# Performance work log

Measured on AMD Instinct MI355X. Metric: run time of the kernel, lower is better.

## Reference

```python
import jax, jax.numpy as jnp
import numpy as np

B, T, C = 4, 2048, 1024
NH = 16
HD = C // NH  # 64


def setup_inputs() -> dict:
    key = jax.random.key(0)
    k1, k2, k3 = jax.random.split(key, 3)
    x = jax.random.normal(k1, (B, T, C), dtype=jnp.float32)
    # causal mask buffer, 1 = keep, 0 = mask out
    mask = jnp.tril(jnp.ones((T, T), dtype=jnp.int32))[None, None, :, :]
    # learned params (Linear with bias=False): torch stores weight as [out, in],
    # y = x @ W.T ; we store transposed for direct matmul
    w_qkv = jax.random.normal(k2, (C, 3 * C), dtype=jnp.float32) / np.sqrt(C)
    w_proj = jax.random.normal(k3, (C, C), dtype=jnp.float32) / np.sqrt(C)
    return {"x": x, "mask": mask, "w_qkv": w_qkv, "w_proj": w_proj}


def reference(x, mask, w_qkv, w_proj):
    b, t, c = x.shape
    qkv = x @ w_qkv  # [b, t, 3c]
    q, k, v = jnp.split(qkv, 3, axis=-1)
    # [b, nh, t, hd]
    q = q.reshape(b, t, NH, HD).transpose(0, 2, 1, 3)
    k = k.reshape(b, t, NH, HD).transpose(0, 2, 1, 3)
    v = v.reshape(b, t, NH, HD).transpose(0, 2, 1, 3)
    att = jnp.einsum("bhqd,bhkd->bhqk", q, k) * (1.0 / np.sqrt(HD))
    att = jnp.where(mask == 0, -jnp.inf, att)
    att = jax.nn.softmax(att, axis=-1)
    y = jnp.einsum("bhqk,bhkd->bhqd", att, v)
    y = y.transpose(0, 2, 1, 3).reshape(b, t, c)
    return y @ w_proj
```

## Files before the change

### kernel.cpp

```cpp
#include <hip/hip_runtime.h>
#include <hip/hip_bf16.h>

typedef _Float16 f16;
typedef __attribute__((ext_vector_type(2))) __fp16 fp16x2;
typedef __attribute__((ext_vector_type(4))) _Float16 f16x4;
typedef __attribute__((ext_vector_type(8))) _Float16 f16x8;
typedef __attribute__((ext_vector_type(4))) float f32x4;

#define MFMA16(a, b, c) __builtin_amdgcn_mfma_f32_16x16x16f16((a), (b), (c), 0, 0, 0)
#define MFMA32(a, b, c) __builtin_amdgcn_mfma_f32_16x16x32_f16((a), (b), (c), 0, 0, 0)
#define EXP2(x) __builtin_amdgcn_exp2f(x)
#define GLOAD_LDS16(g, l)                                                        \
  __builtin_amdgcn_global_load_lds((const __attribute__((address_space(1))) void*)(g), \
                                   (__attribute__((address_space(3))) void*)(l), 16, 0, 0)
typedef const __attribute__((address_space(3))) char* lds_cp;
#define TR16(dst, addr, imm) \
  asm volatile("ds_read_b64_tr_b16 %0, %1 offset:" imm : "=v"(dst) : "v"(addr))

__global__ __launch_bounds__(256) void prep_kernel(
    const float* __restrict__ x, f16* __restrict__ x16,
    const float* __restrict__ wq, f16* __restrict__ wqT,
    const float* __restrict__ wp, f16* __restrict__ wpT) {
  const int blk = blockIdx.x;
  const int tid = threadIdx.x;
  if (blk < 8192) {
    int i = blk * 256 + tid;
    const float4 v = reinterpret_cast<const float4*>(x)[i];
    f16x4 h;
    h[0] = (f16)v.x; h[1] = (f16)v.y; h[2] = (f16)v.z; h[3] = (f16)v.w;
    reinterpret_cast<f16x4*>(x16)[i] = h;
    return;
  }
  const float* src;
  f16* dst;
  int R, Cc, bx, by;
  if (blk < 11264) {
    int j = blk - 8192;
    bx = j % 96; by = j / 96;
    src = wq; dst = wqT; R = 1024; Cc = 3072;
  } else {
    int j = blk - 11264;
    bx = j & 31; by = j >> 5;
    src = wp; dst = wpT; R = 1024; Cc = 1024;
  }
  __shared__ float t[32][33];
  int tx0 = bx * 32, ty0 = by * 32;
  int c = tid & 31;
  int r0 = tid >> 5;
#pragma unroll
  for (int i = 0; i < 4; i++) {
    int r = r0 + 8 * i;
    t[r][c] = src[(size_t)(ty0 + r) * Cc + tx0 + c];
  }
  __syncthreads();
#pragma unroll
  for (int i = 0; i < 4; i++) {
    int a = r0 + 8 * i;
    dst[(size_t)(tx0 + a) * R + ty0 + c] = (f16)t[c][a];
  }
}

__global__ __launch_bounds__(512, 2) void gemm_qkv_kernel(
    const f16* __restrict__ A, const f16* __restrict__ Bt, f16* __restrict__ C,
    int M, int N, int K) {
  __shared__ __align__(16) char smem[163840];
  const int tid = threadIdx.x;
  const int lane = tid & 63, wid = tid >> 6;
  const int wm = wid >> 2, wn = wid & 3;
  const int lo = lane & 15, hi = lane >> 4;

  const int ntn = N / 384;
  const int nwg = (M >> 8) * ntn;
  const int wg = (blockIdx.x & 7) * (nwg >> 3) + (blockIdx.x >> 3);
  const int tm0 = (wg / ntn) << 8;
  const int tn0 = (wg % ntn) * 384;

  const int prow = tid >> 3;
  const int u8 = (tid & 7) ^ (prow & 7);
  const f16* a0 = A + (size_t)(tm0 + prow) * K + u8 * 8;
  const f16* b0 = Bt + (size_t)(tn0 + prow) * K + u8 * 8;

  const int swz = lo & 7;
  const int as0 = (hi ^ swz) << 4, as1 = ((4 + hi) ^ swz) << 4;
  const int abase = (wm * 128 + lo) * 128;
  const int bbase = 32768 + (wn * 96 + lo) * 128;

  f32x4 acc[8][6] = {};

  auto stage = [&](int ke, char* buf) {
#pragma unroll
    for (int c = 0; c < 4; c++)
      GLOAD_LDS16(a0 + (size_t)c * 64 * K + ke, buf + c * 8192 + tid * 16);
#pragma unroll
    for (int c = 0; c < 6; c++)
      GLOAD_LDS16(b0 + (size_t)c * 64 * K + ke, buf + 32768 + c * 8192 + tid * 16);
  };

  const int NT = K >> 6;
  stage(0, smem);

  for (int t = 0; t < NT; t++) {
    char* db = smem + (t & 1) * 81920;
    asm volatile("s_waitcnt vmcnt(0)" ::: "memory");
    __builtin_amdgcn_s_barrier();
    if (t + 1 < NT) stage((t + 1) << 6, smem + ((t + 1) & 1) * 81920);
    __builtin_amdgcn_sched_barrier(0);

#pragma unroll
    for (int ks = 0; ks < 2; ks++) {
      const int so = ks ? as1 : as0;
      f16x8 b[6];
#pragma unroll
      for (int ni = 0; ni < 6; ni++)
        b[ni] = *(const f16x8*)(db + bbase + ni * 2048 + so);
      __builtin_amdgcn_s_setprio(1);
#pragma unroll
      for (int mi = 0; mi < 8; mi++) {
        f16x8 a = *(const f16x8*)(db + abase + mi * 2048 + so);
#pragma unroll
        for (int ni = 0; ni < 6; ni++)
          acc[mi][ni] = MFMA32(a, b[ni], acc[mi][ni]);
      }
      __builtin_amdgcn_s_setprio(0);
    }
  }

#pragma unroll
  for (int mi = 0; mi < 8; mi++)
#pragma unroll
    for (int ni = 0; ni < 6; ni++)
#pragma unroll
      for (int r = 0; r < 4; r++) {
        int row = tm0 + wm * 128 + mi * 16 + 4 * hi + r;
        int col = tn0 + wn * 96 + ni * 16 + lo;
        C[(size_t)row * N + col] = (f16)acc[mi][ni][r];
      }
}

template <bool OUT_F32>
__global__ __launch_bounds__(512, 2) void gemm_deep_kernel(
    const f16* __restrict__ A, const f16* __restrict__ Bt, void* __restrict__ Cout,
    int M, int N, int K) {
  __shared__ __align__(16) char smem[147456];
  const int tid = threadIdx.x;
  const int lane = tid & 63, wid = tid >> 6;
  const int wm = wid >> 2, wn = wid & 3;
  const int lo = lane & 15, hi = lane >> 4;

  const int ntn = N >> 7;
  const int nwg = (M >> 8) * ntn;
  const int wg = (blockIdx.x & 7) * (nwg >> 3) + (blockIdx.x >> 3);
  const int tm0 = (wg / ntn) << 8;
  const int tn0 = (wg % ntn) << 7;

  const int prow = tid >> 3;
  const int u8 = (tid & 7) ^ (prow & 7);
  const f16* asrc[4];
  const f16* bsrc[2];
#pragma unroll
  for (int c = 0; c < 4; c++) asrc[c] = A + (size_t)(tm0 + c * 64 + prow) * K + u8 * 8;
#pragma unroll
  for (int c = 0; c < 2; c++) bsrc[c] = Bt + (size_t)(tn0 + c * 64 + prow) * K + u8 * 8;

  const int swz = lo & 7;
  const int s0 = (hi ^ swz) << 4, s1 = ((4 + hi) ^ swz) << 4;
  const int abase0 = wm * 16384 + lo * 128 + s0;
  const int abase1 = wm * 16384 + lo * 128 + s1;
  int boff0[2], boff1[2];
#pragma unroll
  for (int ni = 0; ni < 2; ni++) {
    int g = 2 * wn + ni;
    int base = 32768 + (g >> 2) * 8192 + ((g & 3) * 16 + lo) * 128;
    boff0[ni] = base + s0;
    boff1[ni] = base + s1;
  }

  f32x4 acc[8][2] = {};

  auto stage = [&](int kt, char* buf) {
    const int ke = kt << 6;
#pragma unroll
    for (int c = 0; c < 4; c++)
      GLOAD_LDS16(asrc[c] + ke, buf + c * 8192 + tid * 16);
#pragma unroll
    for (int c = 0; c < 2; c++)
      GLOAD_LDS16(bsrc[c] + ke, buf + 32768 + c * 8192 + tid * 16);
  };

  const int NT = K >> 6;
  stage(0, smem);
  stage(1, smem + 49152);

  int bufi = 0;
  for (int t = 0; t < NT; t++) {
    char* db = smem + bufi * 49152;
    if (t + 1 < NT) {
      asm volatile("s_waitcnt vmcnt(6)" ::: "memory");
    } else {
      asm volatile("s_waitcnt vmcnt(0)" ::: "memory");
    }
    __builtin_amdgcn_s_barrier();
    if (t + 2 < NT) {
      int nb = bufi + 2;
      if (nb >= 3) nb -= 3;
      stage(t + 2, smem + nb * 49152);
    }
    __builtin_amdgcn_sched_barrier(0);

    f16x8 a[8][2], b[2][2];
#pragma unroll
    for (int mi = 0; mi < 8; mi++) {
      int off = (mi >> 2) * 8192 + (mi & 3) * 2048;
      a[mi][0] = *(const f16x8*)(db + abase0 + off);
      a[mi][1] = *(const f16x8*)(db + abase1 + off);
    }
#pragma unroll
    for (int ni = 0; ni < 2; ni++) {
      b[ni][0] = *(const f16x8*)(db + boff0[ni]);
      b[ni][1] = *(const f16x8*)(db + boff1[ni]);
    }
    __builtin_amdgcn_s_setprio(1);
#pragma unroll
    for (int mi = 0; mi < 8; mi++)
#pragma unroll
      for (int ni = 0; ni < 2; ni++) {
        acc[mi][ni] = MFMA32(a[mi][0], b[ni][0], acc[mi][ni]);
        acc[mi][ni] = MFMA32(a[mi][1], b[ni][1], acc[mi][ni]);
      }
    __builtin_amdgcn_s_setprio(0);

    bufi = (bufi == 2) ? 0 : bufi + 1;
  }

#pragma unroll
  for (int mi = 0; mi < 8; mi++)
#pragma unroll
    for (int ni = 0; ni < 2; ni++)
#pragma unroll
      for (int r = 0; r < 4; r++) {
        int row = tm0 + wm * 128 + mi * 16 + 4 * hi + r;
        int col = tn0 + wn * 32 + ni * 16 + lo;
        float v = acc[mi][ni][r];
        if (OUT_F32)
          ((float*)Cout)[(size_t)row * N + col] = v;
        else
          ((f16*)Cout)[(size_t)row * N + col] = (f16)v;
      }
}

__global__ __launch_bounds__(512, 2) void attn_kernel(
    const f16* __restrict__ qkv, f16* __restrict__ y) {
  constexpr int T = 2048, NHD = 3072, LDO = 72;
  const int bh = blockIdx.x;
  const int b = bh >> 4, h = bh & 15;
  const int pr = blockIdx.y;
  const int tid = threadIdx.x;
  const int lane = tid & 63, w = tid >> 6;
  const int lo = lane & 15, hi = lane >> 4;

  const size_t base = (size_t)b * T * NHD + (size_t)h * 64;
  const f16* Qp = qkv + base;
  const f16* Kp = qkv + base + 1024;
  const f16* Vp = qkv + base + 2048;

  __shared__ __align__(16) char smem[32768];
  f16 (*Ol)[LDO] = (f16(*)[LDO])smem;

  const int mytile = (w < 4) ? pr : (31 - pr);
  const int qb = mytile * 64 + (w & 3) * 16;

  const float scf = 0.125f * 1.44269504089f;
  f16x8 qf[2];
  {
    const f16* qrow = Qp + (size_t)(qb + lo) * NHD;
#pragma unroll
    for (int ks = 0; ks < 2; ks++) {
      f16x8 v = *(const f16x8*)&qrow[ks * 32 + 8 * hi];
#pragma unroll
      for (int j = 0; j < 8; j++) v[j] = (f16)((float)v[j] * scf);
      qf[ks] = v;
    }
  }

  f32x4 oacc[4] = {};
  f32x4 lacc = {};
  const f16x4 ones4 = {(f16)1.f, (f16)1.f, (f16)1.f, (f16)1.f};

  const int kr = tid >> 3;
  const int kslot = (tid & 7) ^ (kr & 7);
  const int vkey = 4 * ((tid & 127) >> 3) + ((tid >> 1) & 3);
  const int vcol = (tid >> 7) * 16 + (tid & 1) * 8;

  const int kfo0 = lo * 64 + ((hi ^ (lo & 7)) * 8);
  const int kfo1 = lo * 64 + (((4 + hi) ^ (lo & 7)) * 8);

  auto stage = [&](int kv, int c) {
    char* kb = smem + c * 8192;
    char* vb = smem + 16384 + c * 8192;
    GLOAD_LDS16(&Kp[(size_t)(kv + kr) * NHD + kslot * 8], kb + tid * 16);
    GLOAD_LDS16(&Vp[(size_t)(kv + vkey) * NHD + vcol], vb + tid * 16);
  };

  const int nt = 32 - pr;
  stage(0, 0);
  asm volatile("s_waitcnt vmcnt(0)" ::: "memory");
  __builtin_amdgcn_s_barrier();

  for (int t = 0; t < nt; t++) {
    const int cur = t & 1;
    const int kv0 = t * 64;
    if (t + 1 < nt) stage(kv0 + 64, cur ^ 1);

    if (kv0 <= qb + 15) {
      const f16* Kl = (const f16*)(smem + cur * 8192);
      f16x8 kf0[4], kf1[4];
#pragma unroll
      for (int ct = 0; ct < 4; ct++) {
        kf0[ct] = *(const f16x8*)&Kl[ct * 1024 + kfo0];
        kf1[ct] = *(const f16x8*)&Kl[ct * 1024 + kfo1];
      }
      f32x4 s_[4] = {};
      __builtin_amdgcn_s_setprio(1);
#pragma unroll
      for (int ct = 0; ct < 4; ct++) s_[ct] = MFMA32(kf0[ct], qf[0], s_[ct]);
#pragma unroll
      for (int ct = 0; ct < 4; ct++) s_[ct] = MFMA32(kf1[ct], qf[1], s_[ct]);
      __builtin_amdgcn_s_setprio(0);

      lds_cp vtrb = (lds_cp)(smem + 16384 + cur * 8192) + lane * 8;
      f16x4 v[4][4];
#pragma unroll
      for (int ct = 0; ct < 4; ct++) {
        lds_cp bct = vtrb + ct * 2048;
        TR16(v[ct][0], bct, "0");
        TR16(v[ct][1], bct, "512");
        TR16(v[ct][2], bct, "1024");
        TR16(v[ct][3], bct, "1536");
      }

      if (kv0 + 63 > qb) {
        const int q = qb + lo;
#pragma unroll
        for (int ct = 0; ct < 4; ct++)
#pragma unroll
          for (int r = 0; r < 4; r++)
            if (kv0 + ct * 16 + 4 * hi + r > q) s_[ct][r] = -3.0e38f;
      }
      f16x4 pb[4];
#pragma unroll
      for (int ct = 0; ct < 4; ct++) {
        float p0 = EXP2(s_[ct][0]), p1 = EXP2(s_[ct][1]);
        float p2 = EXP2(s_[ct][2]), p3 = EXP2(s_[ct][3]);
        union { f16x4 vv; fp16x2 hh[2]; } u;
        u.hh[0] = __builtin_amdgcn_cvt_pkrtz(p0, p1);
        u.hh[1] = __builtin_amdgcn_cvt_pkrtz(p2, p3);
        pb[ct] = u.vv;
      }
      __builtin_amdgcn_s_setprio(1);
#pragma unroll
      for (int kk = 0; kk < 4; kk++) lacc = MFMA16(ones4, pb[kk], lacc);
      __builtin_amdgcn_s_setprio(0);

      asm volatile("s_waitcnt lgkmcnt(0)" ::: "memory");
      __builtin_amdgcn_sched_barrier(0);
      __builtin_amdgcn_s_setprio(1);
#pragma unroll
      for (int ct = 0; ct < 4; ct++) {
        oacc[ct] = MFMA16(v[ct][0], pb[0], oacc[ct]);
        oacc[ct] = MFMA16(v[ct][1], pb[1], oacc[ct]);
        oacc[ct] = MFMA16(v[ct][2], pb[2], oacc[ct]);
        oacc[ct] = MFMA16(v[ct][3], pb[3], oacc[ct]);
      }
      __builtin_amdgcn_s_setprio(0);
    }

    asm volatile("s_waitcnt vmcnt(0)" ::: "memory");
    __builtin_amdgcn_s_barrier();
  }

  const float inv = 1.f / lacc[0];
#pragma unroll
  for (int ct = 0; ct < 4; ct++) {
    f16x4 o4;
#pragma unroll
    for (int r = 0; r < 4; r++) o4[r] = (f16)(oacc[ct][r] * inv);
    *(f16x4*)&Ol[w * 16 + lo][ct * 16 + 4 * hi] = o4;
  }
  __syncthreads();
#pragma unroll
  for (int i = 0; i < 2; i++) {
    int idx = tid + 512 * i;
    int qq = idx >> 3, ch = idx & 7;
    int row = ((qq < 64) ? pr : (31 - pr)) * 64 + (qq & 63);
    *(f16x8*)&y[((size_t)b * T + row) * 1024 + (size_t)h * 64 + ch * 8] =
        *(const f16x8*)&Ol[qq][ch * 8];
  }
}

extern "C" void kernel_launch(void* const* d_in, const int* in_sizes, int n_in,
                              void* d_out, int out_size, void* d_ws, size_t ws_size,
                              hipStream_t stream) {
  const float* x = (const float*)d_in[0];
  const float* w_qkv = (const float*)d_in[2];
  const float* w_proj = (const float*)d_in[3];

  constexpr int B = 4, T = 2048, C = 1024, NH = 16;
  constexpr int M = B * T;
  constexpr int N1 = 3 * C;

  char* ws = (char*)d_ws;
  f16* x16 = (f16*)ws;    ws += (size_t)M * C * 2;
  f16* wqkvT = (f16*)ws;  ws += (size_t)N1 * C * 2;
  f16* wprojT = (f16*)ws; ws += (size_t)C * C * 2;
  f16* qkvb = (f16*)ws;   ws += (size_t)M * N1 * 2;
  f16* y16 = (f16*)ws;

  prep_kernel<<<12288, 256, 0, stream>>>(x, x16, w_qkv, wqkvT, w_proj, wprojT);
  gemm_qkv_kernel<<<(M / 256) * (N1 / 384), 512, 0, stream>>>(x16, wqkvT, qkvb, M, N1, C);
  attn_kernel<<<dim3(B * NH, 16), 512, 0, stream>>>(qkvb, y16);
  gemm_deep_kernel<true><<<(M / 256) * (C / 128), 512, 0, stream>>>(y16, wprojT, (float*)d_out, M, C, C);
}
```

Measured before the change: 144.0 us.

## Retile projection GEMM to 128x128 and double KV tile per attention iteration

The projection GEMM drops the 512-thread, 256x128 triple-buffered kernel for a 256-thread, 128x128-tile double-buffered kernel with a 4x4 MFMA block per wave. This gives more workgroups (512 instead of 256) on the 1024-wide output. The attention kernel now stages 128 keys per loop iteration instead of 64 and processes two 64-key halves inside. This halves the number of barriers and load-issue points but doubles LDS use to 64KB, which may limit occupancy. The GEMM also loses its deeper prefetch, since it waits with vmcnt(0) every iteration.

```diff
diff --git a/kernel.cpp b/kernel.cpp
--- a/kernel.cpp
+++ b/kernel.cpp
@@ -137,114 +137,84 @@
       }
 }
 
-template <bool OUT_F32>
-__global__ __launch_bounds__(512, 2) void gemm_deep_kernel(
-    const f16* __restrict__ A, const f16* __restrict__ Bt, void* __restrict__ Cout,
+__global__ __launch_bounds__(256, 2) void gemm_proj_kernel(
+    const f16* __restrict__ A, const f16* __restrict__ Bt, float* __restrict__ C,
     int M, int N, int K) {
-  __shared__ __align__(16) char smem[147456];
+  __shared__ __align__(16) char smem[65536];
   const int tid = threadIdx.x;
   const int lane = tid & 63, wid = tid >> 6;
-  const int wm = wid >> 2, wn = wid & 3;
+  const int wm = wid >> 1, wn = wid & 1;
   const int lo = lane & 15, hi = lane >> 4;
 
   const int ntn = N >> 7;
-  const int nwg = (M >> 8) * ntn;
+  const int nwg = (M >> 7) * ntn;
   const int wg = (blockIdx.x & 7) * (nwg >> 3) + (blockIdx.x >> 3);
-  const int tm0 = (wg / ntn) << 8;
+  const int tm0 = (wg / ntn) << 7;
   const int tn0 = (wg % ntn) << 7;
 
-  const int prow = tid >> 3;
-  const int u8 = (tid & 7) ^ (prow & 7);
   const f16* asrc[4];
-  const f16* bsrc[2];
-#pragma unroll
-  for (int c = 0; c < 4; c++) asrc[c] = A + (size_t)(tm0 + c * 64 + prow) * K + u8 * 8;
-#pragma unroll
-  for (int c = 0; c < 2; c++) bsrc[c] = Bt + (size_t)(tn0 + c * 64 + prow) * K + u8 * 8;
+  const f16* bsrc[4];
+#pragma unroll
+  for (int i = 0; i < 4; i++) {
+    int L = tid + 256 * i;
+    int prow = L >> 3, u = (L & 7) ^ (prow & 7);
+    asrc[i] = A + (size_t)(tm0 + prow) * K + u * 8;
+    bsrc[i] = Bt + (size_t)(tn0 + prow) * K + u * 8;
+  }
 
   const int swz = lo & 7;
-  const int s0 = (hi ^ swz) << 4, s1 = ((4 + hi) ^ swz) << 4;
-  const int abase0 = wm * 16384 + lo * 128 + s0;
-  const int abase1 = wm * 16384 + lo * 128 + s1;
-  int boff0[2], boff1[2];
-#pragma unroll
-  for (int ni = 0; ni < 2; ni++) {
-    int g = 2 * wn + ni;
-    int base = 32768 + (g >> 2) * 8192 + ((g & 3) * 16 + lo) * 128;
-    boff0[ni] = base + s0;
-    boff1[ni] = base + s1;
-  }
-
-  f32x4 acc[8][2] = {};
-
-  auto stage = [&](int kt, char* buf) {
-    const int ke = kt << 6;
-#pragma unroll
-    for (int c = 0; c < 4; c++)
-      GLOAD_LDS16(asrc[c] + ke, buf + c * 8192 + tid * 16);
-#pragma unroll
-    for (int c = 0; c < 2; c++)
-      GLOAD_LDS16(bsrc[c] + ke, buf + 32768 + c * 8192 + tid * 16);
+  const int as0 = (hi ^ swz) << 4, as1 = ((4 + hi) ^ swz) << 4;
+  const int abase = (wm * 64 + lo) * 128;
+  const int bbase = 16384 + (wn * 64 + lo) * 128;
+
+  f32x4 acc[4][4] = {};
+
+  auto stage = [&](int ke, char* buf) {
+#pragma unroll
+    for (int i = 0; i < 4; i++)
+      GLOAD_LDS16(asrc[i] + ke, buf + (tid + 256 * i) * 16);
+#pragma unroll
+    for (int i = 0; i < 4; i++)
+      GLOAD_LDS16(bsrc[i] + ke, buf + 16384 + (tid + 256 * i) * 16);
   };
 
   const int NT = K >> 6;
   stage(0, smem);
-  stage(1, smem + 49152);
-
-  int bufi = 0;
+
   for (int t = 0; t < NT; t++) {
-    char* db = smem + bufi * 49152;
-    if (t + 1 < NT) {
-      asm volatile("s_waitcnt vmcnt(6)" ::: "memory");
-    } else {
-      asm volatile("s_waitcnt vmcnt(0)" ::: "memory");
+    char* db = smem + (t & 1) * 32768;
+    asm volatile("s_waitcnt vmcnt(0)" ::: "memory");
+    __builtin_amdgcn_s_barrier();
+    if (t + 1 < NT) stage((t + 1) << 6, smem + ((t + 1) & 1) * 32768);
+    __builtin_amdgcn_sched_barrier(0);
+
+#pragma unroll
+    for (int ks = 0; ks < 2; ks++) {
+      const int so = ks ? as1 : as0;
+      f16x8 a[4], b[4];
+#pragma unroll
+      for (int mi = 0; mi < 4; mi++) a[mi] = *(const f16x8*)(db + abase + mi * 2048 + so);
+#pragma unroll
+      for (int ni = 0; ni < 4; ni++) b[ni] = *(const f16x8*)(db + bbase + ni * 2048 + so);
+      __builtin_amdgcn_s_setprio(1);
+#pragma unroll
+      for (int mi = 0; mi < 4; mi++)
+#pragma unroll
+        for (int ni = 0; ni < 4; ni++)
+          acc[mi][ni] = MFMA32(a[mi], b[ni], acc[mi][ni]);
+      __builtin_amdgcn_s_setprio(0);
     }
-    __builtin_amdgcn_s_barrier();
-    if (t + 2 < NT) {
-      int nb = bufi + 2;
-      if (nb >= 3) nb -= 3;
-      stage(t + 2, smem + nb * 49152);
-    }
-    __builtin_amdgcn_sched_barrier(0);
-
-    f16x8 a[8][2], b[2][2];
-#pragma unroll
-    for (int mi = 0; mi < 8; mi++) {
-      int off = (mi >> 2) * 8192 + (mi & 3) * 2048;
-      a[mi][0] = *(const f16x8*)(db + abase0 + off);
-      a[mi][1] = *(const f16x8*)(db + abase1 + off);
-    }
-#pragma unroll
-    for (int ni = 0; ni < 2; ni++) {
-      b[ni][0] = *(const f16x8*)(db + boff0[ni]);
-      b[ni][1] = *(const f16x8*)(db + boff1[ni]);
-    }
-    __builtin_amdgcn_s_setprio(1);
-#pragma unroll
-    for (int mi = 0; mi < 8; mi++)
-#pragma unroll
-      for (int ni = 0; ni < 2; ni++) {
-        acc[mi][ni] = MFMA32(a[mi][0], b[ni][0], acc[mi][ni]);
-        acc[mi][ni] = MFMA32(a[mi][1], b[ni][1], acc[mi][ni]);
-      }
-    __builtin_amdgcn_s_setprio(0);
-
-    bufi = (bufi == 2) ? 0 : bufi + 1;
-  }
-
-#pragma unroll
-  for (int mi = 0; mi < 8; mi++)
-#pragma unroll
-    for (int ni = 0; ni < 2; ni++)
+  }
+
+#pragma unroll
+  for (int mi = 0; mi < 4; mi++)
+#pragma unroll
+    for (int ni = 0; ni < 4; ni++)
 #pragma unroll
       for (int r = 0; r < 4; r++) {
-        int row = tm0 + wm * 128 + mi * 16 + 4 * hi + r;
-        int col = tn0 + wn * 32 + ni * 16 + lo;
-        float v = acc[mi][ni][r];
-        if (OUT_F32)
-          ((float*)Cout)[(size_t)row * N + col] = v;
-        else
-          ((f16*)Cout)[(size_t)row * N + col] = (f16)v;
+        int row = tm0 + wm * 64 + mi * 16 + 4 * hi + r;
+        int col = tn0 + wn * 64 + ni * 16 + lo;
+        C[(size_t)row * N + col] = acc[mi][ni][r];
       }
 }
 
@@ -263,7 +233,7 @@
   const f16* Kp = qkv + base + 1024;
   const f16* Vp = qkv + base + 2048;
 
-  __shared__ __align__(16) char smem[32768];
+  __shared__ __align__(16) char smem[65536];
   f16 (*Ol)[LDO] = (f16(*)[LDO])smem;
 
   const int mytile = (w < 4) ? pr : (31 - pr);
@@ -295,24 +265,29 @@
   const int kfo1 = lo * 64 + (((4 + hi) ^ (lo & 7)) * 8);
 
   auto stage = [&](int kv, int c) {
-    char* kb = smem + c * 8192;
-    char* vb = smem + 16384 + c * 8192;
+    char* kb = smem + c * 16384;
+    char* vb = smem + 32768 + c * 16384;
     GLOAD_LDS16(&Kp[(size_t)(kv + kr) * NHD + kslot * 8], kb + tid * 16);
+    GLOAD_LDS16(&Kp[(size_t)(kv + kr + 64) * NHD + kslot * 8], kb + 8192 + tid * 16);
     GLOAD_LDS16(&Vp[(size_t)(kv + vkey) * NHD + vcol], vb + tid * 16);
+    GLOAD_LDS16(&Vp[(size_t)(kv + 64 + vkey) * NHD + vcol], vb + 8192 + tid * 16);
   };
 
-  const int nt = 32 - pr;
+  const int nt = (33 - pr) >> 1;
   stage(0, 0);
   asm volatile("s_waitcnt vmcnt(0)" ::: "memory");
   __builtin_amdgcn_s_barrier();
 
   for (int t = 0; t < nt; t++) {
     const int cur = t & 1;
-    const int kv0 = t * 64;
-    if (t + 1 < nt) stage(kv0 + 64, cur ^ 1);
-
-    if (kv0 <= qb + 15) {
-      const f16* Kl = (const f16*)(smem + cur * 8192);
+    if (t + 1 < nt) stage((t + 1) * 128, cur ^ 1);
+
+#pragma unroll
+    for (int half = 0; half < 2; half++) {
+      const int kv0 = t * 128 + half * 64;
+      if (kv0 > qb + 15) continue;
+
+      const f16* Kl = (const f16*)(smem + cur * 16384 + half * 8192);
       f16x8 kf0[4], kf1[4];
 #pragma unroll
       for (int ct = 0; ct < 4; ct++) {
@@ -327,7 +302,7 @@
       for (int ct = 0; ct < 4; ct++) s_[ct] = MFMA32(kf1[ct], qf[1], s_[ct]);
       __builtin_amdgcn_s_setprio(0);
 
-      lds_cp vtrb = (lds_cp)(smem + 16384 + cur * 8192) + lane * 8;
+      lds_cp vtrb = (lds_cp)(smem + 32768 + cur * 16384 + half * 8192) + lane * 8;
       f16x4 v[4][4];
 #pragma unroll
       for (int ct = 0; ct < 4; ct++) {
@@ -418,5 +393,5 @@
   prep_kernel<<<12288, 256, 0, stream>>>(x, x16, w_qkv, wqkvT, w_proj, wprojT);
   gemm_qkv_kernel<<<(M / 256) * (N1 / 384), 512, 0, stream>>>(x16, wqkvT, qkvb, M, N1, C);
   attn_kernel<<<dim3(B * NH, 16), 512, 0, stream>>>(qkvb, y16);
-  gemm_deep_kernel<true><<<(M / 256) * (C / 128), 512, 0, stream>>>(y16, wprojT, (float*)d_out, M, C, C);
-}
+  gemm_proj_kernel<<<(M / 128) * (C / 128), 256, 0, stream>>>(y16, wprojT, (float*)d_out, M, C, C);
+}
```

Result: no change. 146.3 us (+1.6%).

## Process both paired query tiles per wave to reuse K/V fragments

Applied to the files above, without the earlier changes.

The attention block drops from 512 to 256 threads, and each wave now handles two 16-row query slices, one from the early tile and one from the mirrored late tile. The K fragments and transposed V reads loaded from LDS are reused for both slices, which halves LDS reads per query row. Each thread now issues two global-to-LDS loads per operand per stage. The early-tile path is skipped under causal masking once it goes fully inactive. Register pressure rises from the doubled accumulators and score arrays, and the launch bounds now allow 4 blocks per CU, which may cost occupancy or cause spills.

```diff
diff --git a/kernel.cpp b/kernel.cpp
--- a/kernel.cpp
+++ b/kernel.cpp
@@ -248,7 +248,7 @@
       }
 }
 
-__global__ __launch_bounds__(512, 2) void attn_kernel(
+__global__ __launch_bounds__(256, 4) void attn_kernel(
     const f16* __restrict__ qkv, f16* __restrict__ y) {
   constexpr int T = 2048, NHD = 3072, LDO = 72;
   const int bh = blockIdx.x;
@@ -266,29 +266,31 @@
   __shared__ __align__(16) char smem[32768];
   f16 (*Ol)[LDO] = (f16(*)[LDO])smem;
 
-  const int mytile = (w < 4) ? pr : (31 - pr);
-  const int qb = mytile * 64 + (w & 3) * 16;
+  const int qb0 = pr * 64 + w * 16;
+  const int qb1 = (31 - pr) * 64 + w * 16;
 
   const float scf = 0.125f * 1.44269504089f;
-  f16x8 qf[2];
-  {
-    const f16* qrow = Qp + (size_t)(qb + lo) * NHD;
+  f16x8 qf[2][2];
+#pragma unroll
+  for (int s = 0; s < 2; s++) {
+    const f16* qrow = Qp + (size_t)((s ? qb1 : qb0) + lo) * NHD;
 #pragma unroll
     for (int ks = 0; ks < 2; ks++) {
       f16x8 v = *(const f16x8*)&qrow[ks * 32 + 8 * hi];
 #pragma unroll
       for (int j = 0; j < 8; j++) v[j] = (f16)((float)v[j] * scf);
-      qf[ks] = v;
-    }
-  }
-
-  f32x4 oacc[4] = {};
-  f32x4 lacc = {};
+      qf[s][ks] = v;
+    }
+  }
+
+  f32x4 oacc[2][4] = {};
+  f32x4 lacc[2] = {};
   const f16x4 ones4 = {(f16)1.f, (f16)1.f, (f16)1.f, (f16)1.f};
 
   const int kr = tid >> 3;
   const int kslot = (tid & 7) ^ (kr & 7);
-  const int vkey = 4 * ((tid & 127) >> 3) + ((tid >> 1) & 3);
+  const int tp = tid & 127;
+  const int vkey = 4 * (tp >> 3) + ((tid >> 1) & 3);
   const int vcol = (tid >> 7) * 16 + (tid & 1) * 8;
 
   const int kfo0 = lo * 64 + ((hi ^ (lo & 7)) * 8);
@@ -298,7 +300,9 @@
     char* kb = smem + c * 8192;
     char* vb = smem + 16384 + c * 8192;
     GLOAD_LDS16(&Kp[(size_t)(kv + kr) * NHD + kslot * 8], kb + tid * 16);
+    GLOAD_LDS16(&Kp[(size_t)(kv + kr + 32) * NHD + kslot * 8], kb + 4096 + tid * 16);
     GLOAD_LDS16(&Vp[(size_t)(kv + vkey) * NHD + vcol], vb + tid * 16);
+    GLOAD_LDS16(&Vp[(size_t)(kv + vkey) * NHD + vcol + 32], vb + 4096 + tid * 16);
   };
 
   const int nt = 32 - pr;
@@ -311,85 +315,133 @@
     const int kv0 = t * 64;
     if (t + 1 < nt) stage(kv0 + 64, cur ^ 1);
 
-    if (kv0 <= qb + 15) {
-      const f16* Kl = (const f16*)(smem + cur * 8192);
-      f16x8 kf0[4], kf1[4];
+    const f16* Kl = (const f16*)(smem + cur * 8192);
+    const bool act0 = kv0 <= qb0 + 15;
+
+    f16x8 kf0[4], kf1[4];
+#pragma unroll
+    for (int ct = 0; ct < 4; ct++) {
+      kf0[ct] = *(const f16x8*)&Kl[ct * 1024 + kfo0];
+      kf1[ct] = *(const f16x8*)&Kl[ct * 1024 + kfo1];
+    }
+
+    f32x4 s1_[4] = {};
+    __builtin_amdgcn_s_setprio(1);
+#pragma unroll
+    for (int ct = 0; ct < 4; ct++) s1_[ct] = MFMA32(kf0[ct], qf[1][0], s1_[ct]);
+#pragma unroll
+    for (int ct = 0; ct < 4; ct++) s1_[ct] = MFMA32(kf1[ct], qf[1][1], s1_[ct]);
+    __builtin_amdgcn_s_setprio(0);
+    f32x4 s0_[4] = {};
+    if (act0) {
+      __builtin_amdgcn_s_setprio(1);
+#pragma unroll
+      for (int ct = 0; ct < 4; ct++) s0_[ct] = MFMA32(kf0[ct], qf[0][0], s0_[ct]);
+#pragma unroll
+      for (int ct = 0; ct < 4; ct++) s0_[ct] = MFMA32(kf1[ct], qf[0][1], s0_[ct]);
+      __builtin_amdgcn_s_setprio(0);
+    }
+
+    lds_cp vtrb = (lds_cp)(smem + 16384 + cur * 8192) + lane * 8;
+    f16x4 v[4][4];
+#pragma unroll
+    for (int ct = 0; ct < 4; ct++) {
+      lds_cp bct = vtrb + ct * 2048;
+      TR16(v[ct][0], bct, "0");
+      TR16(v[ct][1], bct, "512");
+      TR16(v[ct][2], bct, "1024");
+      TR16(v[ct][3], bct, "1536");
+    }
+
+    f16x4 pb1[4];
+    {
+      if (kv0 + 63 > qb1) {
+        const int q = qb1 + lo;
+#pragma unroll
+        for (int ct = 0; ct < 4; ct++)
+#pragma unroll
+          for (int r = 0; r < 4; r++)
+            if (kv0 + ct * 16 + 4 * hi + r > q) s1_[ct][r] = -3.0e38f;
+      }
 #pragma unroll
       for (int ct = 0; ct < 4; ct++) {
-        kf0[ct] = *(const f16x8*)&Kl[ct * 1024 + kfo0];
-        kf1[ct] = *(const f16x8*)&Kl[ct * 1024 + kfo1];
-      }
-      f32x4 s_[4] = {};
-      __builtin_amdgcn_s_setprio(1);
-#pragma unroll
-      for (int ct = 0; ct < 4; ct++) s_[ct] = MFMA32(kf0[ct], qf[0], s_[ct]);
-#pragma unroll
-      for (int ct = 0; ct < 4; ct++) s_[ct] = MFMA32(kf1[ct], qf[1], s_[ct]);
-      __builtin_amdgcn_s_setprio(0);
-
-      lds_cp vtrb = (lds_cp)(smem + 16384 + cur * 8192) + lane * 8;
-      f16x4 v[4][4];
-#pragma unroll
-      for (int ct = 0; ct < 4; ct++) {
-        lds_cp bct = vtrb + ct * 2048;
-        TR16(v[ct][0], bct, "0");
-        TR16(v[ct][1], bct, "512");
-        TR16(v[ct][2], bct, "1024");
-        TR16(v[ct][3], bct, "1536");
-      }
-
-      if (kv0 + 63 > qb) {
-        const int q = qb + lo;
-#pragma unroll
-        for (int ct = 0; ct < 4; ct++)
-#pragma unroll
-          for (int r = 0; r < 4; r++)
-            if (kv0 + ct * 16 + 4 * hi + r > q) s_[ct][r] = -3.0e38f;
-      }
-      f16x4 pb[4];
-#pragma unroll
-      for (int ct = 0; ct < 4; ct++) {
-        float p0 = EXP2(s_[ct][0]), p1 = EXP2(s_[ct][1]);
-        float p2 = EXP2(s_[ct][2]), p3 = EXP2(s_[ct][3]);
+        float p0 = EXP2(s1_[ct][0]), p1 = EXP2(s1_[ct][1]);
+        float p2 = EXP2(s1_[ct][2]), p3 = EXP2(s1_[ct][3]);
         union { f16x4 vv; fp16x2 hh[2]; } u;
         u.hh[0] = __builtin_amdgcn_cvt_pkrtz(p0, p1);
         u.hh[1] = __builtin_amdgcn_cvt_pkrtz(p2, p3);
-        pb[ct] = u.vv;
+        pb1[ct] = u.vv;
       }
       __builtin_amdgcn_s_setprio(1);
 #pragma unroll
-      for (int kk = 0; kk < 4; kk++) lacc = MFMA16(ones4, pb[kk], lacc);
+      for (int kk = 0; kk < 4; kk++) lacc[1] = MFMA16(ones4, pb1[kk], lacc[1]);
       __builtin_amdgcn_s_setprio(0);
-
-      asm volatile("s_waitcnt lgkmcnt(0)" ::: "memory");
-      __builtin_amdgcn_sched_barrier(0);
+    }
+    f16x4 pb0[4];
+    if (act0) {
+      if (kv0 + 63 > qb0) {
+        const int q = qb0 + lo;
+#pragma unroll
+        for (int ct = 0; ct < 4; ct++)
+#pragma unroll
+          for (int r = 0; r < 4; r++)
+            if (kv0 + ct * 16 + 4 * hi + r > q) s0_[ct][r] = -3.0e38f;
+      }
+#pragma unroll
+      for (int ct = 0; ct < 4; ct++) {
+        float p0 = EXP2(s0_[ct][0]), p1 = EXP2(s0_[ct][1]);
+        float p2 = EXP2(s0_[ct][2]), p3 = EXP2(s0_[ct][3]);
+        union { f16x4 vv; fp16x2 hh[2]; } u;
+        u.hh[0] = __builtin_amdgcn_cvt_pkrtz(p0, p1);
+        u.hh[1] = __builtin_amdgcn_cvt_pkrtz(p2, p3);
+        pb0[ct] = u.vv;
+      }
       __builtin_amdgcn_s_setprio(1);
 #pragma unroll
+      for (int kk = 0; kk < 4; kk++) lacc[0] = MFMA16(ones4, pb0[kk], lacc[0]);
+      __builtin_amdgcn_s_setprio(0);
+    }
+
+    asm volatile("s_waitcnt lgkmcnt(0)" ::: "memory");
+    __builtin_amdgcn_sched_barrier(0);
+    __builtin_amdgcn_s_setprio(1);
+#pragma unroll
+    for (int ct = 0; ct < 4; ct++) {
+      oacc[1][ct] = MFMA16(v[ct][0], pb1[0], oacc[1][ct]);
+      oacc[1][ct] = MFMA16(v[ct][1], pb1[1], oacc[1][ct]);
+      oacc[1][ct] = MFMA16(v[ct][2], pb1[2], oacc[1][ct]);
+      oacc[1][ct] = MFMA16(v[ct][3], pb1[3], oacc[1][ct]);
+    }
+    if (act0) {
+#pragma unroll
       for (int ct = 0; ct < 4; ct++) {
-        oacc[ct] = MFMA16(v[ct][0], pb[0], oacc[ct]);
-        oacc[ct] = MFMA16(v[ct][1], pb[1], oacc[ct]);
-        oacc[ct] = MFMA16(v[ct][2], pb[2], oacc[ct]);
-        oacc[ct] = MFMA16(v[ct][3], pb[3], oacc[ct]);
-      }
-      __builtin_amdgcn_s_setprio(0);
-    }
+        oacc[0][ct] = MFMA16(v[ct][0], pb0[0], oacc[0][ct]);
+        oacc[0][ct] = MFMA16(v[ct][1], pb0[1], oacc[0][ct]);
+        oacc[0][ct] = MFMA16(v[ct][2], pb0[2], oacc[0][ct]);
+        oacc[0][ct] = MFMA16(v[ct][3], pb0[3], oacc[0][ct]);
+      }
+    }
+    __builtin_amdgcn_s_setprio(0);
 
     asm volatile("s_waitcnt vmcnt(0)" ::: "memory");
     __builtin_amdgcn_s_barrier();
   }
 
-  const float inv = 1.f / lacc[0];
-#pragma unroll
-  for (int ct = 0; ct < 4; ct++) {
-    f16x4 o4;
-#pragma unroll
-    for (int r = 0; r < 4; r++) o4[r] = (f16)(oacc[ct][r] * inv);
-    *(f16x4*)&Ol[w * 16 + lo][ct * 16 + 4 * hi] = o4;
+#pragma unroll
+  for (int s = 0; s < 2; s++) {
+    const float inv = 1.f / lacc[s][0];
+#pragma unroll
+    for (int ct = 0; ct < 4; ct++) {
+      f16x4 o4;
+#pragma unroll
+      for (int r = 0; r < 4; r++) o4[r] = (f16)(oacc[s][ct][r] * inv);
+      *(f16x4*)&Ol[s * 64 + w * 16 + lo][ct * 16 + 4 * hi] = o4;
+    }
   }
   __syncthreads();
 #pragma unroll
-  for (int i = 0; i < 2; i++) {
-    int idx = tid + 512 * i;
+  for (int i = 0; i < 4; i++) {
+    int idx = tid + 256 * i;
     int qq = idx >> 3, ch = idx & 7;
     int row = ((qq < 64) ? pr : (31 - pr)) * 64 + (qq & 63);
     *(f16x8*)&y[((size_t)b * T + row) * 1024 + (size_t)h * 64 + ch * 8] =
@@ -417,6 +469,6 @@
 
   prep_kernel<<<12288, 256, 0, stream>>>(x, x16, w_qkv, wqkvT, w_proj, wprojT);
   gemm_qkv_kernel<<<(M / 256) * (N1 / 384), 512, 0, stream>>>(x16, wqkvT, qkvb, M, N1, C);
-  attn_kernel<<<dim3(B * NH, 16), 512, 0, stream>>>(qkvb, y16);
+  attn_kernel<<<dim3(B * NH, 16), 256, 0, stream>>>(qkvb, y16);
   gemm_deep_kernel<true><<<(M / 256) * (C / 128), 512, 0, stream>>>(y16, wprojT, (float*)d_out, M, C, C);
 }
```

Result: slower. 169.4 us (+17.7%).
